# Optimization experiments

Hardware: AMD Instinct MI355X
Metric: run time of the kernel (lower is better)

Reference implementation:

```python
import jax, jax.numpy as jnp
import numpy as np

K = 7          # local attention kernel size
PAD = 3        # (K-1)//2 so output spatial dims match input
GROUPS = 8

def unfold2d(x, k):
    # x: [B, C, H+k-1, W+k-1] -> patches [B, C, H, W, k*k] (kh-major, kw-minor, matching F.unfold)
    B, C, Hp, Wp = x.shape
    H, W = Hp - k + 1, Wp - k + 1
    return jnp.stack([x[:, :, i:i + H, j:j + W] for i in range(k) for j in range(k)], axis=-1)

def setup_inputs():
    key = jax.random.key(0)
    k1, k2, k3, k4, k5, k6 = jax.random.split(key, 6)
    B, Cin, H, W = 2, 256, 56, 56
    outc = 256
    scale = (2.0 / Cin) ** 0.5  # kaiming fan_out-ish init
    return {
        "feature_map": jax.random.normal(k1, (B, 2 * Cin, H, W), jnp.float32),
        "w_q": jax.random.normal(k2, (outc, Cin), jnp.float32) * scale,
        "w_k": jax.random.normal(k3, (outc, Cin), jnp.float32) * scale,
        "w_v": jax.random.normal(k4, (outc, Cin), jnp.float32) * scale,
        "rel_h": jax.random.normal(k5, (outc // 2, K), jnp.float32),
        "rel_w": jax.random.normal(k6, (outc // 2, K), jnp.float32),
    }

def reference(feature_map, w_q, w_k, w_v, rel_h, rel_w):
    B, C2, H, W = feature_map.shape
    Cin = C2 // 2
    fm_t0, fm_t1 = feature_map[:, :Cin], feature_map[:, Cin:]
    outc = w_q.shape[0]
    # 1x1 convs (bias=False)
    q = jnp.einsum('oc,bchw->bohw', w_q, fm_t1)                      # [B, outc, H, W]
    padded = jnp.pad(fm_t0, ((0, 0), (0, 0), (PAD, PAD), (PAD, PAD)))
    kk = jnp.einsum('oc,bchw->bohw', w_k, padded)
    vv = jnp.einsum('oc,bchw->bohw', w_v, padded)
    k_out = unfold2d(kk, K)                                          # [B, outc, H, W, K*K]
    v_out = unfold2d(vv, K)
    # relative position bias: first half channels get row bias, second half col bias
    half = outc // 2
    bias_h = jnp.broadcast_to(rel_h[:, :, None], (half, K, K)).reshape(half, K * K)
    bias_w = jnp.broadcast_to(rel_w[:, None, :], (half, K, K)).reshape(half, K * K)
    bias = jnp.concatenate([bias_h, bias_w], axis=0)                 # [outc, K*K]
    k_out = k_out + bias[None, :, None, None, :]
    G, Cg = GROUPS, outc // GROUPS
    qg = q.reshape(B, G, Cg, H, W)
    kg = k_out.reshape(B, G, Cg, H, W, K * K)
    vg = v_out.reshape(B, G, Cg, H, W, K * K)
    logits = jnp.einsum('bgchw,bgchwk->bghwk', qg, kg)
    wts = jax.nn.softmax(logits, axis=-1)
    out = jnp.einsum('bghwk,bgchwk->bgchw', wts, vg)
    return out.reshape(B, outc, H, W)
```

## Files before the change

### kernel.cpp

```cpp
#include <hip/hip_runtime.h>
#include <hip/hip_bf16.h>

#define B    2
#define CIN  256
#define H    56
#define W    56
#define OUTC 256
#define KS   7
#define PAD  3
#define G    8
#define CG   32
#define HP   62
#define WP   62
#define P1   (H * W)
#define P2   (HP * WP)

typedef __attribute__((ext_vector_type(2))) _Float16 h2;
typedef __attribute__((ext_vector_type(8))) _Float16 f16x8;
typedef __attribute__((ext_vector_type(8))) unsigned short ushort8;
typedef __attribute__((ext_vector_type(4))) float f32x4;

__device__ inline unsigned short f2h(float f) {
    const _Float16 h = (_Float16)f;
    return *(const unsigned short*)&h;
}

__device__ inline float fdot2(h2 a, h2 b, float c) {
#if defined(__has_builtin)
#if __has_builtin(__builtin_amdgcn_fdot2)
    return __builtin_amdgcn_fdot2(a, b, c, false);
#else
    return c + (float)a[0] * (float)b[0] + (float)a[1] * (float)b[1];
#endif
#else
    return c + (float)a[0] * (float)b[0] + (float)a[1] * (float)b[1];
#endif
}

#define ASTR 40
__global__ __launch_bounds__(256, 2) void gemm_kernel(const float* __restrict__ fm,
                                                      const float* __restrict__ wq,
                                                      const float* __restrict__ wk,
                                                      const float* __restrict__ wv,
                                                      unsigned short* __restrict__ qi,
                                                      unsigned short* __restrict__ ki,
                                                      unsigned short* __restrict__ vi) {
    const int b = blockIdx.z;
    const bool isQ = blockIdx.y < 2;
    if (isQ && blockIdx.x >= 25) return;
    const int o0 = (isQ ? blockIdx.y : (blockIdx.y - 2)) * 128;
    const int n0 = blockIdx.x * 128;
    const int Nreal = isQ ? P1 : P2;
    const int Pstr  = isQ ? P1 : P2;

    const float* Wsrc;
    int orow0;
    if (isQ)            { Wsrc = wq; orow0 = o0; }
    else if (o0 < 256)  { Wsrc = wk; orow0 = o0; }
    else                { Wsrc = wv; orow0 = o0 - 256; }

    __shared__ unsigned short Alds[128 * ASTR];
    __shared__ unsigned short Blds[128 * ASTR];
    const int tid = threadIdx.x;
    const int lane = tid & 63;
    const int wave = tid >> 6;
    const int wr = (wave >> 1) * 64;
    const int wc = (wave & 1) * 64;
    const int lrow = lane & 15;
    const int quad = lane >> 4;

    const int arow = tid & 127;
    const int akc  = (tid >> 7) * 16;

    const int n = n0 + arow;
    int srcoff = -1;
    if (isQ) {
        if (n < P1) srcoff = n;
    } else {
        if (n < P2) {
            const int y = n / WP, x = n - y * WP;
            const int iy = y - PAD, ix = x - PAD;
            if (iy >= 0 && iy < H && ix >= 0 && ix < W) srcoff = iy * W + ix;
        }
    }
    const float* fmB = fm + ((size_t)b * (2 * CIN) + (isQ ? CIN : 0)) * P1;
    const float* wrow = Wsrc + (size_t)orow0 * CIN + (size_t)arow * CIN + akc;

    unsigned short* alp = Alds + arow * ASTR + akc;
    unsigned short* blp = Blds + arow * ASTR + akc;

    f32x4 acc[4][4] = {};

    float av[16], bv[16];
    {
        const float4 a0 = ((const float4*)wrow)[0];
        const float4 a1 = ((const float4*)wrow)[1];
        const float4 a2 = ((const float4*)wrow)[2];
        const float4 a3 = ((const float4*)wrow)[3];
        av[0]=a0.x; av[1]=a0.y; av[2]=a0.z; av[3]=a0.w;
        av[4]=a1.x; av[5]=a1.y; av[6]=a1.z; av[7]=a1.w;
        av[8]=a2.x; av[9]=a2.y; av[10]=a2.z; av[11]=a2.w;
        av[12]=a3.x; av[13]=a3.y; av[14]=a3.z; av[15]=a3.w;
        #pragma unroll
        for (int j = 0; j < 16; ++j)
            bv[j] = (srcoff >= 0) ? fmB[(size_t)(akc + j) * P1 + srcoff] : 0.f;
    }

    for (int kb = 0; kb < CIN / 32; ++kb) {
        {
            f16x8 p0, p1, p2, p3;
            #pragma unroll
            for (int j = 0; j < 8; ++j) {
                p0[j] = (_Float16)av[j];
                p1[j] = (_Float16)av[8 + j];
                p2[j] = (_Float16)bv[j];
                p3[j] = (_Float16)bv[8 + j];
            }
            *(f16x8*)(alp)     = p0;
            *(f16x8*)(alp + 8) = p1;
            *(f16x8*)(blp)     = p2;
            *(f16x8*)(blp + 8) = p3;
        }
        __syncthreads();
        if (kb < CIN / 32 - 1) {
            const int c0 = (kb + 1) * 32 + akc;
            const float* wnext = wrow + (kb + 1) * 32;
            const float4 a0 = ((const float4*)wnext)[0];
            const float4 a1 = ((const float4*)wnext)[1];
            const float4 a2 = ((const float4*)wnext)[2];
            const float4 a3 = ((const float4*)wnext)[3];
            av[0]=a0.x; av[1]=a0.y; av[2]=a0.z; av[3]=a0.w;
            av[4]=a1.x; av[5]=a1.y; av[6]=a1.z; av[7]=a1.w;
            av[8]=a2.x; av[9]=a2.y; av[10]=a2.z; av[11]=a2.w;
            av[12]=a3.x; av[13]=a3.y; av[14]=a3.z; av[15]=a3.w;
            #pragma unroll
            for (int j = 0; j < 16; ++j)
                bv[j] = (srcoff >= 0) ? fmB[(size_t)(c0 + j) * P1 + srcoff] : 0.f;
        }
        f16x8 af[4], bfr[4];
        #pragma unroll
        for (int mi = 0; mi < 4; ++mi)
            af[mi] = *(const f16x8*)&Alds[(wr + mi * 16 + lrow) * ASTR + quad * 8];
        #pragma unroll
        for (int ni = 0; ni < 4; ++ni)
            bfr[ni] = *(const f16x8*)&Blds[(wc + ni * 16 + lrow) * ASTR + quad * 8];
        #pragma unroll
        for (int mi = 0; mi < 4; ++mi)
            #pragma unroll
            for (int ni = 0; ni < 4; ++ni)
                acc[mi][ni] = __builtin_amdgcn_mfma_f32_16x16x32_f16(af[mi], bfr[ni], acc[mi][ni], 0, 0, 0);
        __syncthreads();
    }

    #pragma unroll
    for (int mi = 0; mi < 4; ++mi) {
        const int gmBase = o0 + wr + mi * 16 + quad * 4;
        int ch0;
        unsigned short* base;
        if (isQ)               { ch0 = gmBase;       base = qi; }
        else if (gmBase < 256) { ch0 = gmBase;       base = ki; }
        else                   { ch0 = gmBase - 256; base = vi; }
        const int g   = ch0 >> 5;
        const int sub = (ch0 >> 3) & 3;
        const int l8  = ch0 & 7;
        unsigned short* pbase = base + ((((size_t)b * 8 + g) * 4 + sub) * Pstr) * 8 + l8;
        #pragma unroll
        for (int ni = 0; ni < 4; ++ni) {
            const int gn = n0 + wc + ni * 16 + lrow;
            if (gn < Nreal) {
                ushort4 pk;
                pk.x = f2h(acc[mi][ni][0]);
                pk.y = f2h(acc[mi][ni][1]);
                pk.z = f2h(acc[mi][ni][2]);
                pk.w = f2h(acc[mi][ni][3]);
                *(ushort4*)(pbase + (size_t)gn * 8) = pk;
            }
        }
    }
}

#define NPOS 496
__global__ __launch_bounds__(128) void attn_kernel(const unsigned short* __restrict__ qi,
                                                   const unsigned short* __restrict__ ki,
                                                   const unsigned short* __restrict__ vi,
                                                   const float* __restrict__ rel_h,
                                                   const float* __restrict__ rel_w,
                                                   float* __restrict__ out) {
    __shared__ f16x8 sbuf[2 * 992];

    const int b  = blockIdx.z;
    const int g  = blockIdx.y;
    const int r0 = blockIdx.x * 2;
    const int oc0 = g * CG;
    const int tid = threadIdx.x;
    const bool active = tid < 112;
    const int rr = tid / 56;
    const int cx = tid - rr * 56;
    const int pix = (r0 + rr) * W + cx;

    const size_t bg4 = ((size_t)b * 8 + g) * 4;
    const size_t rowoff8 = ((size_t)r0 * WP) * 8;

    f16x8* bufA = sbuf;
    f16x8* bufB = sbuf + 992;

    f16x8 qh[4];
    if (active) {
        #pragma unroll
        for (int sub = 0; sub < 4; ++sub)
            qh[sub] = *(const f16x8*)(qi + ((bg4 + sub) * P1 + pix) * 8);
    }

    f16x8 st[8];
    {
        const unsigned short* gb = ki + bg4 * P2 * 8 + rowoff8;
        #pragma unroll
        for (int it = 0; it < 8; ++it) {
            const int e = tid + it * 128;
            if (e < 992) {
                const int sl = (e >= 496);
                const int pos = e - (sl ? 496 : 0);
                st[it] = *(const f16x8*)(gb + ((size_t)sl * P2 + pos) * 8);
            }
        }
        #pragma unroll
        for (int it = 0; it < 8; ++it) {
            const int e = tid + it * 128;
            if (e < 992) bufA[e] = st[it];
        }
    }
    __syncthreads();

    {
        const unsigned short* gb = ki + (bg4 + 2) * P2 * 8 + rowoff8;
        #pragma unroll
        for (int it = 0; it < 8; ++it) {
            const int e = tid + it * 128;
            if (e < 992) {
                const int sl = (e >= 496);
                const int pos = e - (sl ? 496 : 0);
                st[it] = *(const f16x8*)(gb + ((size_t)sl * P2 + pos) * 8);
            }
        }
    }

    float logits[KS * KS];
    if (active) {
        const float* rel = (g < 4) ? (rel_h + oc0 * KS) : (rel_w + (oc0 - 128) * KS);
        float qf[32];
        #pragma unroll
        for (int sub = 0; sub < 4; ++sub)
            #pragma unroll
            for (int j = 0; j < 8; ++j)
                qf[sub * 8 + j] = (float)qh[sub][j];
        float biasdot[KS];
        #pragma unroll
        for (int t = 0; t < KS; ++t) {
            float s = 0.f;
            #pragma unroll
            for (int c = 0; c < 32; ++c) s += qf[c] * rel[c * KS + t];
            biasdot[t] = s;
        }
        #pragma unroll
        for (int i = 0; i < KS; ++i)
            #pragma unroll
            for (int j = 0; j < KS; ++j)
                logits[i * KS + j] = (g < 4) ? biasdot[i] : biasdot[j];

        #pragma unroll
        for (int sl = 0; sl < 2; ++sl) {
            const f16x8 qv = qh[sl];
            const h2 q0 = {qv[0], qv[1]}, q1 = {qv[2], qv[3]};
            const h2 q2 = {qv[4], qv[5]}, q3 = {qv[6], qv[7]};
            #pragma unroll
            for (int i = 0; i < KS; ++i) {
                const int eb = sl * NPOS + (rr + i) * WP + cx;
                #pragma unroll
                for (int j = 0; j < KS; ++j) {
                    const f16x8 kv = bufA[eb + j];
                    float s = logits[i * KS + j];
                    s = fdot2(q0, (h2){kv[0], kv[1]}, s);
                    s = fdot2(q1, (h2){kv[2], kv[3]}, s);
                    s = fdot2(q2, (h2){kv[4], kv[5]}, s);
                    s = fdot2(q3, (h2){kv[6], kv[7]}, s);
                    logits[i * KS + j] = s;
                }
            }
        }
    }
    #pragma unroll
    for (int it = 0; it < 8; ++it) {
        const int e = tid + it * 128;
        if (e < 992) bufB[e] = st[it];
    }
    __syncthreads();

    {
        const unsigned short* gb = vi + bg4 * P2 * 8 + rowoff8;
        #pragma unroll
        for (int it = 0; it < 8; ++it) {
            const int e = tid + it * 128;
            if (e < 992) {
                const int sl = (e >= 496);
                const int pos = e - (sl ? 496 : 0);
                st[it] = *(const f16x8*)(gb + ((size_t)sl * P2 + pos) * 8);
            }
        }
    }

    if (active) {
        #pragma unroll
        for (int sl = 0; sl < 2; ++sl) {
            const f16x8 qv = qh[2 + sl];
            const h2 q0 = {qv[0], qv[1]}, q1 = {qv[2], qv[3]};
            const h2 q2 = {qv[4], qv[5]}, q3 = {qv[6], qv[7]};
            #pragma unroll
            for (int i = 0; i < KS; ++i) {
                const int eb = sl * NPOS + (rr + i) * WP + cx;
                #pragma unroll
                for (int j = 0; j < KS; ++j) {
                    const f16x8 kv = bufB[eb + j];
                    float s = logits[i * KS + j];
                    s = fdot2(q0, (h2){kv[0], kv[1]}, s);
                    s = fdot2(q1, (h2){kv[2], kv[3]}, s);
                    s = fdot2(q2, (h2){kv[4], kv[5]}, s);
                    s = fdot2(q3, (h2){kv[6], kv[7]}, s);
                    logits[i * KS + j] = s;
                }
            }
        }
        float m = logits[0];
        #pragma unroll
        for (int t = 1; t < KS * KS; ++t) m = fmaxf(m, logits[t]);
        float sum = 0.f;
        #pragma unroll
        for (int t = 0; t < KS * KS; ++t) {
            const float e = __expf(logits[t] - m);
            logits[t] = e;
            sum += e;
        }
        const float inv = 1.f / sum;
        #pragma unroll
        for (int t = 0; t < KS * KS; ++t) logits[t] *= inv;
    }
    #pragma unroll
    for (int it = 0; it < 8; ++it) {
        const int e = tid + it * 128;
        if (e < 992) bufA[e] = st[it];
    }
    __syncthreads();

    {
        const unsigned short* gb = vi + (bg4 + 2) * P2 * 8 + rowoff8;
        #pragma unroll
        for (int it = 0; it < 8; ++it) {
            const int e = tid + it * 128;
            if (e < 992) {
                const int sl = (e >= 496);
                const int pos = e - (sl ? 496 : 0);
                st[it] = *(const f16x8*)(gb + ((size_t)sl * P2 + pos) * 8);
            }
        }
    }

    if (active) {
        #pragma unroll
        for (int sl = 0; sl < 2; ++sl) {
            float a[8] = {};
            #pragma unroll
            for (int i = 0; i < KS; ++i) {
                const int eb = sl * NPOS + (rr + i) * WP + cx;
                #pragma unroll
                for (int j = 0; j < KS; ++j) {
                    const f16x8 v = bufA[eb + j];
                    const float wt = logits[i * KS + j];
                    #pragma unroll
                    for (int c = 0; c < 8; ++c) a[c] += wt * (float)v[c];
                }
            }
            float* op = out + ((size_t)b * OUTC + oc0 + sl * 8) * P1 + pix;
            #pragma unroll
            for (int c = 0; c < 8; ++c) op[(size_t)c * P1] = a[c];
        }
    }
    #pragma unroll
    for (int it = 0; it < 8; ++it) {
        const int e = tid + it * 128;
        if (e < 992) bufB[e] = st[it];
    }
    __syncthreads();

    if (active) {
        #pragma unroll
        for (int sl = 0; sl < 2; ++sl) {
            float a[8] = {};
            #pragma unroll
            for (int i = 0; i < KS; ++i) {
                const int eb = sl * NPOS + (rr + i) * WP + cx;
                #pragma unroll
                for (int j = 0; j < KS; ++j) {
                    const f16x8 v = bufB[eb + j];
                    const float wt = logits[i * KS + j];
                    #pragma unroll
                    for (int c = 0; c < 8; ++c) a[c] += wt * (float)v[c];
                }
            }
            float* op = out + ((size_t)b * OUTC + oc0 + 16 + sl * 8) * P1 + pix;
            #pragma unroll
            for (int c = 0; c < 8; ++c) op[(size_t)c * P1] = a[c];
        }
    }
}

extern "C" void kernel_launch(void* const* d_in, const int* in_sizes, int n_in,
                              void* d_out, int out_size, void* d_ws, size_t ws_size,
                              hipStream_t stream) {
    const float* fm = (const float*)d_in[0];
    const float* wq = (const float*)d_in[1];
    const float* wk = (const float*)d_in[2];
    const float* wv = (const float*)d_in[3];
    const float* rh = (const float*)d_in[4];
    const float* rw = (const float*)d_in[5];
    float* out = (float*)d_out;

    unsigned short* ws = (unsigned short*)d_ws;
    unsigned short* qi = ws;
    unsigned short* ki = qi + (size_t)B * OUTC * P1;
    unsigned short* vi = ki + (size_t)B * OUTC * P2;

    gemm_kernel<<<dim3(31, 6, B), 256, 0, stream>>>(fm, wq, wk, wv, qi, ki, vi);
    attn_kernel<<<dim3(H / 2, G, B), 128, 0, stream>>>(qi, ki, vi, rh, rw, out);
}
```

Before: 109.2 us.

## Compute two vertically adjacent output rows per thread to reuse shared K/V loads

Each attn_kernel block now covers four output rows instead of two, and each thread handles two vertically adjacent pixels. A K or V vector read from shared memory is reused for both pixels across the overlapping 7x7 windows, cutting LDS reads per output and the global halo reload per row. The grid shrinks by half, to 224 blocks, and register pressure roughly doubles (two logit arrays, two q sets, 10 staging vectors), which risks spills or lower occupancy.

```diff
diff --git a/kernel.cpp b/kernel.cpp
--- a/kernel.cpp
+++ b/kernel.cpp
@@ -35,6 +35,14 @@
 #else
     return c + (float)a[0] * (float)b[0] + (float)a[1] * (float)b[1];
 #endif
+}
+
+__device__ inline float dot8(const f16x8 q, const f16x8 k, float s) {
+    s = fdot2((h2){q[0], q[1]}, (h2){k[0], k[1]}, s);
+    s = fdot2((h2){q[2], q[3]}, (h2){k[2], k[3]}, s);
+    s = fdot2((h2){q[4], q[5]}, (h2){k[4], k[5]}, s);
+    s = fdot2((h2){q[6], q[7]}, (h2){k[6], k[7]}, s);
+    return s;
 }
 
 #define ASTR 40
@@ -179,54 +187,59 @@
     }
 }
 
-#define NPOS 496
+#define NPOS4 620
+#define HALFE 1240
 __global__ __launch_bounds__(128) void attn_kernel(const unsigned short* __restrict__ qi,
                                                    const unsigned short* __restrict__ ki,
                                                    const unsigned short* __restrict__ vi,
                                                    const float* __restrict__ rel_h,
                                                    const float* __restrict__ rel_w,
                                                    float* __restrict__ out) {
-    __shared__ f16x8 sbuf[2 * 992];
+    __shared__ f16x8 sbuf[2 * HALFE];
 
     const int b  = blockIdx.z;
     const int g  = blockIdx.y;
-    const int r0 = blockIdx.x * 2;
+    const int r0 = blockIdx.x * 4;
     const int oc0 = g * CG;
     const int tid = threadIdx.x;
     const bool active = tid < 112;
-    const int rr = tid / 56;
-    const int cx = tid - rr * 56;
-    const int pix = (r0 + rr) * W + cx;
+    const int rp = tid / 56;
+    const int cx = tid - rp * 56;
+    const int pr0 = r0 + 2 * rp;
+    const int pix0 = pr0 * W + cx;
+    const int pix1 = pix0 + W;
 
     const size_t bg4 = ((size_t)b * 8 + g) * 4;
     const size_t rowoff8 = ((size_t)r0 * WP) * 8;
 
     f16x8* bufA = sbuf;
-    f16x8* bufB = sbuf + 992;
-
-    f16x8 qh[4];
+    f16x8* bufB = sbuf + HALFE;
+
+    f16x8 qh0[4], qh1[4];
     if (active) {
         #pragma unroll
-        for (int sub = 0; sub < 4; ++sub)
-            qh[sub] = *(const f16x8*)(qi + ((bg4 + sub) * P1 + pix) * 8);
-    }
-
-    f16x8 st[8];
+        for (int sub = 0; sub < 4; ++sub) {
+            qh0[sub] = *(const f16x8*)(qi + ((bg4 + sub) * P1 + pix0) * 8);
+            qh1[sub] = *(const f16x8*)(qi + ((bg4 + sub) * P1 + pix1) * 8);
+        }
+    }
+
+    f16x8 st[10];
     {
         const unsigned short* gb = ki + bg4 * P2 * 8 + rowoff8;
         #pragma unroll
-        for (int it = 0; it < 8; ++it) {
+        for (int it = 0; it < 10; ++it) {
             const int e = tid + it * 128;
-            if (e < 992) {
-                const int sl = (e >= 496);
-                const int pos = e - (sl ? 496 : 0);
+            if (e < HALFE) {
+                const int sl = (e >= NPOS4);
+                const int pos = e - (sl ? NPOS4 : 0);
                 st[it] = *(const f16x8*)(gb + ((size_t)sl * P2 + pos) * 8);
             }
         }
         #pragma unroll
-        for (int it = 0; it < 8; ++it) {
+        for (int it = 0; it < 10; ++it) {
             const int e = tid + it * 128;
-            if (e < 992) bufA[e] = st[it];
+            if (e < HALFE) bufA[e] = st[it];
         }
     }
     __syncthreads();
@@ -234,75 +247,77 @@
     {
         const unsigned short* gb = ki + (bg4 + 2) * P2 * 8 + rowoff8;
         #pragma unroll
-        for (int it = 0; it < 8; ++it) {
+        for (int it = 0; it < 10; ++it) {
             const int e = tid + it * 128;
-            if (e < 992) {
-                const int sl = (e >= 496);
-                const int pos = e - (sl ? 496 : 0);
+            if (e < HALFE) {
+                const int sl = (e >= NPOS4);
+                const int pos = e - (sl ? NPOS4 : 0);
                 st[it] = *(const f16x8*)(gb + ((size_t)sl * P2 + pos) * 8);
             }
         }
     }
 
-    float logits[KS * KS];
+    float logits0[KS * KS], logits1[KS * KS];
     if (active) {
         const float* rel = (g < 4) ? (rel_h + oc0 * KS) : (rel_w + (oc0 - 128) * KS);
-        float qf[32];
+        float qf0[32], qf1[32];
         #pragma unroll
         for (int sub = 0; sub < 4; ++sub)
             #pragma unroll
-            for (int j = 0; j < 8; ++j)
-                qf[sub * 8 + j] = (float)qh[sub][j];
-        float biasdot[KS];
+            for (int j = 0; j < 8; ++j) {
+                qf0[sub * 8 + j] = (float)qh0[sub][j];
+                qf1[sub * 8 + j] = (float)qh1[sub][j];
+            }
+        float bd0[KS], bd1[KS];
         #pragma unroll
         for (int t = 0; t < KS; ++t) {
-            float s = 0.f;
-            #pragma unroll
-            for (int c = 0; c < 32; ++c) s += qf[c] * rel[c * KS + t];
-            biasdot[t] = s;
+            float s0 = 0.f, s1 = 0.f;
+            #pragma unroll
+            for (int c = 0; c < 32; ++c) {
+                const float r = rel[c * KS + t];
+                s0 += qf0[c] * r;
+                s1 += qf1[c] * r;
+            }
+            bd0[t] = s0; bd1[t] = s1;
         }
         #pragma unroll
         for (int i = 0; i < KS; ++i)
             #pragma unroll
-            for (int j = 0; j < KS; ++j)
-                logits[i * KS + j] = (g < 4) ? biasdot[i] : biasdot[j];
-
-        #pragma unroll
-        for (int sl = 0; sl < 2; ++sl) {
-            const f16x8 qv = qh[sl];
-            const h2 q0 = {qv[0], qv[1]}, q1 = {qv[2], qv[3]};
-            const h2 q2 = {qv[4], qv[5]}, q3 = {qv[6], qv[7]};
-            #pragma unroll
-            for (int i = 0; i < KS; ++i) {
-                const int eb = sl * NPOS + (rr + i) * WP + cx;
+            for (int j = 0; j < KS; ++j) {
+                logits0[i * KS + j] = (g < 4) ? bd0[i] : bd0[j];
+                logits1[i * KS + j] = (g < 4) ? bd1[i] : bd1[j];
+            }
+
+        #pragma unroll
+        for (int s = 0; s < 2; ++s) {
+            const f16x8 q0 = qh0[s];
+            const f16x8 q1 = qh1[s];
+            #pragma unroll
+            for (int j = 0; j < KS; ++j) {
                 #pragma unroll
-                for (int j = 0; j < KS; ++j) {
-                    const f16x8 kv = bufA[eb + j];
-                    float s = logits[i * KS + j];
-                    s = fdot2(q0, (h2){kv[0], kv[1]}, s);
-                    s = fdot2(q1, (h2){kv[2], kv[3]}, s);
-                    s = fdot2(q2, (h2){kv[4], kv[5]}, s);
-                    s = fdot2(q3, (h2){kv[6], kv[7]}, s);
-                    logits[i * KS + j] = s;
+                for (int ii = 0; ii < 8; ++ii) {
+                    const f16x8 kv = bufA[s * NPOS4 + (2 * rp + ii) * WP + cx + j];
+                    if (ii < 7)  logits0[ii * KS + j]       = dot8(q0, kv, logits0[ii * KS + j]);
+                    if (ii >= 1) logits1[(ii - 1) * KS + j] = dot8(q1, kv, logits1[(ii - 1) * KS + j]);
                 }
             }
         }
     }
     #pragma unroll
-    for (int it = 0; it < 8; ++it) {
+    for (int it = 0; it < 10; ++it) {
         const int e = tid + it * 128;
-        if (e < 992) bufB[e] = st[it];
+        if (e < HALFE) bufB[e] = st[it];
     }
     __syncthreads();
 
     {
         const unsigned short* gb = vi + bg4 * P2 * 8 + rowoff8;
         #pragma unroll
-        for (int it = 0; it < 8; ++it) {
+        for (int it = 0; it < 10; ++it) {
             const int e = tid + it * 128;
-            if (e < 992) {
-                const int sl = (e >= 496);
-                const int pos = e - (sl ? 496 : 0);
+            if (e < HALFE) {
+                const int sl = (e >= NPOS4);
+                const int pos = e - (sl ? NPOS4 : 0);
                 st[it] = *(const f16x8*)(gb + ((size_t)sl * P2 + pos) * 8);
             }
         }
@@ -310,54 +325,65 @@
 
     if (active) {
         #pragma unroll
-        for (int sl = 0; sl < 2; ++sl) {
-            const f16x8 qv = qh[2 + sl];
-            const h2 q0 = {qv[0], qv[1]}, q1 = {qv[2], qv[3]};
-            const h2 q2 = {qv[4], qv[5]}, q3 = {qv[6], qv[7]};
-            #pragma unroll
-            for (int i = 0; i < KS; ++i) {
-                const int eb = sl * NPOS + (rr + i) * WP + cx;
+        for (int s = 0; s < 2; ++s) {
+            const f16x8 q0 = qh0[2 + s];
+            const f16x8 q1 = qh1[2 + s];
+            #pragma unroll
+            for (int j = 0; j < KS; ++j) {
                 #pragma unroll
-                for (int j = 0; j < KS; ++j) {
-                    const f16x8 kv = bufB[eb + j];
-                    float s = logits[i * KS + j];
-                    s = fdot2(q0, (h2){kv[0], kv[1]}, s);
-                    s = fdot2(q1, (h2){kv[2], kv[3]}, s);
-                    s = fdot2(q2, (h2){kv[4], kv[5]}, s);
-                    s = fdot2(q3, (h2){kv[6], kv[7]}, s);
-                    logits[i * KS + j] = s;
+                for (int ii = 0; ii < 8; ++ii) {
+                    const f16x8 kv = bufB[s * NPOS4 + (2 * rp + ii) * WP + cx + j];
+                    if (ii < 7)  logits0[ii * KS + j]       = dot8(q0, kv, logits0[ii * KS + j]);
+                    if (ii >= 1) logits1[(ii - 1) * KS + j] = dot8(q1, kv, logits1[(ii - 1) * KS + j]);
                 }
             }
         }
-        float m = logits[0];
-        #pragma unroll
-        for (int t = 1; t < KS * KS; ++t) m = fmaxf(m, logits[t]);
-        float sum = 0.f;
-        #pragma unroll
-        for (int t = 0; t < KS * KS; ++t) {
-            const float e = __expf(logits[t] - m);
-            logits[t] = e;
-            sum += e;
-        }
-        const float inv = 1.f / sum;
-        #pragma unroll
-        for (int t = 0; t < KS * KS; ++t) logits[t] *= inv;
+        {
+            float m = logits0[0];
+            #pragma unroll
+            for (int t = 1; t < KS * KS; ++t) m = fmaxf(m, logits0[t]);
+            float sum = 0.f;
+            #pragma unroll
+            for (int t = 0; t < KS * KS; ++t) {
+                const float e = __expf(logits0[t] - m);
+                logits0[t] = e;
+                sum += e;
+            }
+            const float inv = 1.f / sum;
+            #pragma unroll
+            for (int t = 0; t < KS * KS; ++t) logits0[t] *= inv;
+        }
+        {
+            float m = logits1[0];
+            #pragma unroll
+            for (int t = 1; t < KS * KS; ++t) m = fmaxf(m, logits1[t]);
+            float sum = 0.f;
+            #pragma unroll
+            for (int t = 0; t < KS * KS; ++t) {
+                const float e = __expf(logits1[t] - m);
+                logits1[t] = e;
+                sum += e;
+            }
+            const float inv = 1.f / sum;
+            #pragma unroll
+            for (int t = 0; t < KS * KS; ++t) logits1[t] *= inv;
+        }
     }
     #pragma unroll
-    for (int it = 0; it < 8; ++it) {
+    for (int it = 0; it < 10; ++it) {
         const int e = tid + it * 128;
-        if (e < 992) bufA[e] = st[it];
+        if (e < HALFE) bufA[e] = st[it];
     }
     __syncthreads();
 
     {
         const unsigned short* gb = vi + (bg4 + 2) * P2 * 8 + rowoff8;
         #pragma unroll
-        for (int it = 0; it < 8; ++it) {
+        for (int it = 0; it < 10; ++it) {
             const int e = tid + it * 128;
-            if (e < 992) {
-                const int sl = (e >= 496);
-                const int pos = e - (sl ? 496 : 0);
+            if (e < HALFE) {
+                const int sl = (e >= NPOS4);
+                const int pos = e - (sl ? NPOS4 : 0);
                 st[it] = *(const f16x8*)(gb + ((size_t)sl * P2 + pos) * 8);
             }
         }
@@ -365,49 +391,69 @@
 
     if (active) {
         #pragma unroll
-        for (int sl = 0; sl < 2; ++sl) {
-            float a[8] = {};
-            #pragma unroll
-            for (int i = 0; i < KS; ++i) {
-                const int eb = sl * NPOS + (rr + i) * WP + cx;
+        for (int s = 0; s < 2; ++s) {
+            float a0[8] = {}, a1[8] = {};
+            #pragma unroll
+            for (int j = 0; j < KS; ++j) {
                 #pragma unroll
-                for (int j = 0; j < KS; ++j) {
-                    const f16x8 v = bufA[eb + j];
-                    const float wt = logits[i * KS + j];
-                    #pragma unroll
-                    for (int c = 0; c < 8; ++c) a[c] += wt * (float)v[c];
+                for (int ii = 0; ii < 8; ++ii) {
+                    const f16x8 v = bufA[s * NPOS4 + (2 * rp + ii) * WP + cx + j];
+                    if (ii < 7) {
+                        const float wt = logits0[ii * KS + j];
+                        #pragma unroll
+                        for (int c = 0; c < 8; ++c) a0[c] += wt * (float)v[c];
+                    }
+                    if (ii >= 1) {
+                        const float wt = logits1[(ii - 1) * KS + j];
+                        #pragma unroll
+                        for (int c = 0; c < 8; ++c) a1[c] += wt * (float)v[c];
+                    }
                 }
             }
-            float* op = out + ((size_t)b * OUTC + oc0 + sl * 8) * P1 + pix;
-            #pragma unroll
-            for (int c = 0; c < 8; ++c) op[(size_t)c * P1] = a[c];
+            float* op0 = out + ((size_t)b * OUTC + oc0 + s * 8) * P1 + pix0;
+            float* op1 = out + ((size_t)b * OUTC + oc0 + s * 8) * P1 + pix1;
+            #pragma unroll
+            for (int c = 0; c < 8; ++c) {
+                op0[(size_t)c * P1] = a0[c];
+                op1[(size_t)c * P1] = a1[c];
+            }
         }
     }
     #pragma unroll
-    for (int it = 0; it < 8; ++it) {
+    for (int it = 0; it < 10; ++it) {
         const int e = tid + it * 128;
-        if (e < 992) bufB[e] = st[it];
+        if (e < HALFE) bufB[e] = st[it];
     }
     __syncthreads();
 
     if (active) {
         #pragma unroll
-        for (int sl = 0; sl < 2; ++sl) {
-            float a[8] = {};
-            #pragma unroll
-            for (int i = 0; i < KS; ++i) {
-                const int eb = sl * NPOS + (rr + i) * WP + cx;
+        for (int s = 0; s < 2; ++s) {
+            float a0[8] = {}, a1[8] = {};
+            #pragma unroll
+            for (int j = 0; j < KS; ++j) {
                 #pragma unroll
-                for (int j = 0; j < KS; ++j) {
-                    const f16x8 v = bufB[eb + j];
-                    const float wt = logits[i * KS + j];
-                    #pragma unroll
-                    for (int c = 0; c < 8; ++c) a[c] += wt * (float)v[c];
+                for (int ii = 0; ii < 8; ++ii) {
+                    const f16x8 v = bufB[s * NPOS4 + (2 * rp + ii) * WP + cx + j];
+                    if (ii < 7) {
+                        const float wt = logits0[ii * KS + j];
+                        #pragma unroll
+                        for (int c = 0; c < 8; ++c) a0[c] += wt * (float)v[c];
+                    }
+                    if (ii >= 1) {
+                        const float wt = logits1[(ii - 1) * KS + j];
+                        #pragma unroll
+                        for (int c = 0; c < 8; ++c) a1[c] += wt * (float)v[c];
+                    }
                 }
             }
-            float* op = out + ((size_t)b * OUTC + oc0 + 16 + sl * 8) * P1 + pix;
-            #pragma unroll
-            for (int c = 0; c < 8; ++c) op[(size_t)c * P1] = a[c];
+            float* op0 = out + ((size_t)b * OUTC + oc0 + 16 + s * 8) * P1 + pix0;
+            float* op1 = out + ((size_t)b * OUTC + oc0 + 16 + s * 8) * P1 + pix1;
+            #pragma unroll
+            for (int c = 0; c < 8; ++c) {
+                op0[(size_t)c * P1] = a0[c];
+                op1[(size_t)c * P1] = a1[c];
+            }
         }
     }
 }
@@ -429,5 +475,5 @@
     unsigned short* vi = ki + (size_t)B * OUTC * P2;
 
     gemm_kernel<<<dim3(31, 6, B), 256, 0, stream>>>(fm, wq, wk, wv, qi, ki, vi);
-    attn_kernel<<<dim3(H / 2, G, B), 128, 0, stream>>>(qi, ki, vi, rh, rw, out);
-}
+    attn_kernel<<<dim3(H / 4, G, B), 128, 0, stream>>>(qi, ki, vi, rh, rw, out);
+}
```

New measurement: 104.9 us. 3.9% less time.
